# Optimization experiments

Hardware: AMD Instinct MI355X
Metric: run time of the kernel (lower is better)

The kernel has to match this reference:

```python
import jax, jax.numpy as jnp
import numpy as np

B, IN, H, NB = 8192, 1024, 2048, 8
BS = H // NB  # 256


def setup_inputs() -> dict:
    key = jax.random.key(0)
    ks = jax.random.split(key, 4)
    s = 0.02
    return {
        "x": jax.random.normal(ks[0], (B, IN), dtype=jnp.float32),
        "h": jax.random.normal(ks[1], (B, H), dtype=jnp.float32),
        "W_ir": jax.random.normal(ks[2], (3 * H, IN), dtype=jnp.float32) * s,
        "b_ir_lin": jnp.zeros((3 * H,), dtype=jnp.float32),
        "b_ir": jnp.zeros((3 * H,), dtype=jnp.float32),
        "W_h": jax.random.normal(ks[3], (NB, 3 * BS, BS), dtype=jnp.float32) * s,
        "b_hr": jnp.zeros((3 * H,), dtype=jnp.float32),
    }


def reference(x, h, W_ir, b_ir_lin, b_ir, W_h, b_hr):
    b = x.shape[0]
    nb, three_bs, bs = W_h.shape
    hdim = nb * bs
    # input projection: w_ir(x) + b_ir  -> [B, 3H], chunked globally into r,z,n
    wx = x @ W_ir.T + b_ir_lin + b_ir
    wxr, wxz, wxn = jnp.split(wx, 3, axis=1)
    wxr = wxr.reshape(b, nb, bs)
    wxz = wxz.reshape(b, nb, bs)
    wxn = wxn.reshape(b, nb, bs)
    # block-diagonal hidden projection: per-block Linear(bs -> 3*bs), no bias
    hb = h.reshape(b, nb, bs)
    # b_hr is sliced in contiguous chunks of 3*bs per block (local r,z,n layout)
    wh = jnp.einsum('bki,koi->bko', hb, W_h) + b_hr.reshape(nb, three_bs)
    whr, whz, whn = jnp.split(wh, 3, axis=2)
    r = jax.nn.sigmoid(wxr + whr)
    z = jax.nn.sigmoid(wxz + whz)
    n = jnp.tanh(wxn + r * whn)
    h_new = (1.0 - z) * hb + z * n
    return h_new.reshape(b, hdim)
```

## Files before the change

### kernel.cpp

```cpp
#include <hip/hip_runtime.h>
#include <cstdint>
#include <cstddef>


typedef __attribute__((ext_vector_type(8))) short bf16x8;
typedef __attribute__((ext_vector_type(4))) float f32x4;

__device__ __forceinline__ unsigned short f2bf(float f) {
    uint32_t u = __float_as_uint(f);
    u += 0x7FFFu + ((u >> 16) & 1u);
    return (unsigned short)(u >> 16);
}

__device__ __forceinline__ void gload16(const void* g, void* l) {
    __builtin_amdgcn_global_load_lds(
        (const __attribute__((address_space(1))) void*)g,
        (__attribute__((address_space(3))) void*)l,
        16, 0, 0);
}

__device__ __forceinline__ float sigmoidf_(float x) {
    return 1.0f / (1.0f + __expf(-x));
}
__device__ __forceinline__ float tanhf_(float x) {
    float e = __expf(-2.0f * fabsf(x));
    float t = (1.0f - e) / (1.0f + e);
    return copysignf(t, x);
}

__global__ __launch_bounds__(256)
void cast_f32_to_bf16(const float* __restrict__ s, unsigned short* __restrict__ d, int n4) {
    int i = blockIdx.x * 256 + threadIdx.x;
    if (i >= n4) return;
    const float4 v = *reinterpret_cast<const float4*>(s + (size_t)i * 4);
    ushort4 o;
    o.x = f2bf(v.x); o.y = f2bf(v.y); o.z = f2bf(v.z); o.w = f2bf(v.w);
    *reinterpret_cast<ushort4*>(d + (size_t)i * 4) = o;
}


#define MFMA12(mb, NT) do {                                                    \
    asm volatile("s_waitcnt lgkmcnt(0)" ::: "memory");                         \
    __builtin_amdgcn_sched_barrier(0);                                         \
    __builtin_amdgcn_s_setprio(1);                                             \
    _Pragma("unroll")                                                          \
    for (int m_ = 0; m_ < 4; ++m_) {                                           \
        acc[0][(mb) + m_] = __builtin_amdgcn_mfma_f32_16x16x32_bf16(           \
            av[m_], bv[0], acc[0][(mb) + m_], 0, 0, 0);                        \
        acc[1][(mb) + m_] = __builtin_amdgcn_mfma_f32_16x16x32_bf16(           \
            av[m_], bv[1], acc[1][(mb) + m_], 0, 0, 0);                        \
        acc[NT][(mb) + m_] = __builtin_amdgcn_mfma_f32_16x16x32_bf16(          \
            av[m_], bv[2], acc[NT][(mb) + m_], 0, 0, 0);                       \
    }                                                                          \
    __builtin_amdgcn_s_setprio(0);                                             \
} while (0)

#define LDA(m, kb_) (*(const bf16x8*)(aS + (wm * 128 + (m) * 16 + fr) * 64 + (kb_)))
#define LDB(s, kb_) (*(const bf16x8*)(bS + ((s) * 64 + wn * 16 + fr) * 64 + (kb_)))

#define IB1(kt, ds) do {                                                       \
    gload16(b1[0] + (size_t)(kt) * 64, Bs + (ds) * 12288 + doff);              \
    gload16(b1[1] + (size_t)(kt) * 64, Bs + (ds) * 12288 + 4096 + doff);       \
    gload16(b1[2] + (size_t)(kt) * 64, Bs + (ds) * 12288 + 8192 + doff); } while (0)
#define IA1a(kt, ds) do {                                                      \
    gload16(a1[0] + (size_t)(kt) * 64, As + (ds) * 16384 + doff);              \
    gload16(a1[2] + (size_t)(kt) * 64, As + (ds) * 16384 + 8192 + doff); } while (0)
#define IA1b(kt, ds) do {                                                      \
    gload16(a1[1] + (size_t)(kt) * 64, As + (ds) * 16384 + 4096 + doff);       \
    gload16(a1[3] + (size_t)(kt) * 64, As + (ds) * 16384 + 12288 + doff); } while (0)
#define IB2(k2, ds) do {                                                       \
    gload16(b2[0] + (size_t)(k2) * 64, Bs + (ds) * 12288 + doff);              \
    gload16(b2[1] + (size_t)(k2) * 64, Bs + (ds) * 12288 + 4096 + doff);       \
    gload16(b2[2] + (size_t)(k2) * 64, Bs + (ds) * 12288 + 8192 + doff); } while (0)
#define IA2a(k2, ds) do {                                                      \
    gload16(a2[0] + (size_t)(k2) * 64, As + (ds) * 16384 + doff);              \
    gload16(a2[2] + (size_t)(k2) * 64, As + (ds) * 16384 + 8192 + doff); } while (0)
#define IA2b(k2, ds) do {                                                      \
    gload16(a2[1] + (size_t)(k2) * 64, As + (ds) * 16384 + 4096 + doff);       \
    gload16(a2[3] + (size_t)(k2) * 64, As + (ds) * 16384 + 12288 + doff); } while (0)

#define KSTEP(slot_, I0, W0, I1, W1, I2, NT) do {                              \
    const unsigned short* aS = As + (slot_) * 16384;                           \
    const unsigned short* bS = Bs + (slot_) * 12288;                           \
    I0;                                                                        \
    asm volatile("s_waitcnt vmcnt(" W0 ")" ::: "memory");                      \
    __builtin_amdgcn_s_barrier();                                              \
    _Pragma("unroll") for (int m_ = 0; m_ < 4; ++m_) av[m_] = LDA(m_, kb0);    \
    _Pragma("unroll") for (int s_ = 0; s_ < 3; ++s_) bv[s_] = LDB(s_, kb0);    \
    MFMA12(0, NT);                                                             \
    I1;                                                                        \
    asm volatile("s_waitcnt vmcnt(" W1 ")" ::: "memory");                      \
    __builtin_amdgcn_s_barrier();                                              \
    _Pragma("unroll") for (int m_ = 0; m_ < 4; ++m_) av[m_] = LDA(4 + m_, kb0);\
    MFMA12(4, NT);                                                             \
    I2;                                                                        \
    _Pragma("unroll") for (int m_ = 0; m_ < 4; ++m_) av[m_] = LDA(m_, kb1);    \
    _Pragma("unroll") for (int s_ = 0; s_ < 3; ++s_) bv[s_] = LDB(s_, kb1);    \
    MFMA12(0, NT);                                                             \
    _Pragma("unroll") for (int m_ = 0; m_ < 4; ++m_) av[m_] = LDA(4 + m_, kb1);\
    MFMA12(4, NT);                                                             \
    __builtin_amdgcn_s_barrier();                                              \
} while (0)

__global__ __launch_bounds__(512, 2)
void gru_fused(const unsigned short* __restrict__ Xb,
               const unsigned short* __restrict__ Wirb,
               const unsigned short* __restrict__ Hbb,
               const unsigned short* __restrict__ Whb,
               const float* __restrict__ b_ir_lin,
               const float* __restrict__ b_ir,
               const float* __restrict__ b_hr,
               const float* __restrict__ Hf,
               float* __restrict__ out) {
    constexpr int K1 = 1024, H = 2048;
    __shared__ unsigned short lds[2 * 16384 + 2 * 12288];
    unsigned short* const As = lds;
    unsigned short* const Bs = lds + 2 * 16384;

    const int tid  = threadIdx.x;
    const int lane = tid & 63;
    const int w    = tid >> 6;
    const int wm   = w >> 2;
    const int wn   = w & 3;

    const int bid  = blockIdx.x;
    const int kb   = bid & 7;
    const int idx  = bid >> 3;
    const int bm   = (idx >> 2) * 256;
    const int hsub = idx & 3;
    const int hcb  = kb * 256 + hsub * 64;

    const int srow  = tid >> 3;
    const int chunk = (tid & 7) ^ (srow & 7);
    const int scol  = chunk * 8;
    const int doff  = tid * 8;
    const unsigned short* a1[4];
    const unsigned short* a2[4];
    #pragma unroll
    for (int s = 0; s < 4; ++s) {
        a1[s] = Xb  + (size_t)(bm + s * 64 + srow) * K1 + scol;
        a2[s] = Hbb + (size_t)(bm + s * 64 + srow) * H + kb * 256 + scol;
    }
    const unsigned short* b1[3];
    const unsigned short* b2[3];
    #pragma unroll
    for (int s = 0; s < 3; ++s) {
        b1[s] = Wirb + (size_t)(s * 2048 + hcb + srow) * K1 + scol;
        b2[s] = Whb + (size_t)kb * 196608 + (size_t)(s * 256 + hsub * 64 + srow) * 256 + scol;
    }

    const int fr  = lane & 15;
    const int k0e = (lane >> 4) * 8;
    const int mfr = (fr & 7) << 4;
    const int kb0 = ((k0e * 2) ^ mfr) >> 1;
    const int kb1 = (((k0e * 2) + 64) ^ mfr) >> 1;

    f32x4 acc[4][8] = {};
    bf16x8 av[4], bv[3];

    IB1(0, 0); IA1a(0, 0); IA1b(0, 0);

    #pragma unroll 1
    for (int t = 0; t < 15; ++t) {
        const int sl = t & 1, nx = sl ^ 1;
        KSTEP(sl, IB1(t + 1, nx), "5", IA1a(t + 1, nx), "5", IA1b(t + 1, nx), 2);
    }
    KSTEP(1, IB2(0, 0), "5", IA2a(0, 0), "5", IA2b(0, 0), 2);
    #pragma unroll 1
    for (int t = 16; t < 19; ++t) {
        const int sl = t & 1, nx = sl ^ 1;
        KSTEP(sl, IB2(t - 15, nx), "5", IA2a(t - 15, nx), "5", IA2b(t - 15, nx), 3);
    }
    KSTEP(1, ((void)0), "2", ((void)0), "0", ((void)0), 3);

    const int rq   = (lane >> 4) * 4;
    const int hcol = hcb + wn * 16 + fr;
    const int lcol = hcol & 255;
    const float bir0 = b_ir_lin[hcol]        + b_ir[hcol];
    const float bir1 = b_ir_lin[2048 + hcol] + b_ir[2048 + hcol];
    const float bir2 = b_ir_lin[4096 + hcol] + b_ir[4096 + hcol];
    const float bhr0 = b_hr[kb * 768 + lcol];
    const float bhr1 = b_hr[kb * 768 + 256 + lcol];
    const float bhr2 = b_hr[kb * 768 + 512 + lcol];
    #pragma unroll
    for (int mi = 0; mi < 8; ++mi) {
        #pragma unroll
        for (int r = 0; r < 4; ++r) {
            const int row = bm + wm * 128 + mi * 16 + rq + r;
            const float pr = acc[0][mi][r] + bir0 + bhr0;
            const float pz = acc[1][mi][r] + bir1 + bhr1;
            const float xn = acc[2][mi][r] + bir2;
            const float hn = acc[3][mi][r] + bhr2;
            const float rg = sigmoidf_(pr);
            const float zg = sigmoidf_(pz);
            const float ng = tanhf_(xn + rg * hn);
            const float hv = Hf[(size_t)row * H + hcol];
            out[(size_t)row * H + hcol] = (1.0f - zg) * hv + zg * ng;
        }
    }
}

extern "C" void kernel_launch(void* const* d_in, const int* in_sizes, int n_in,
                              void* d_out, int out_size, void* d_ws, size_t ws_size,
                              hipStream_t stream) {
    const float* x        = (const float*)d_in[0];
    const float* h        = (const float*)d_in[1];
    const float* W_ir     = (const float*)d_in[2];
    const float* b_ir_lin = (const float*)d_in[3];
    const float* b_ir     = (const float*)d_in[4];
    const float* W_h      = (const float*)d_in[5];
    const float* b_hr     = (const float*)d_in[6];
    float* out = (float*)d_out;

    char* ws = (char*)d_ws;
    unsigned short* xb   = (unsigned short*)(ws);
    unsigned short* wirb = (unsigned short*)(ws + 16777216);
    unsigned short* hb   = (unsigned short*)(ws + 29360128);
    unsigned short* whb  = (unsigned short*)(ws + 62914560);

    cast_f32_to_bf16<<<8192,  256, 0, stream>>>(x,    xb,   2097152);
    cast_f32_to_bf16<<<6144,  256, 0, stream>>>(W_ir, wirb, 1572864);
    cast_f32_to_bf16<<<16384, 256, 0, stream>>>(h,    hb,   4194304);
    cast_f32_to_bf16<<<1536,  256, 0, stream>>>(W_h,  whb,  393216);

    gru_fused<<<1024, 512, 0, stream>>>(xb, wirb, hb, whb,
                                        b_ir_lin, b_ir, b_hr, h, out);
}
```

Measured before the change: 182.1 us.

## Halve fused GRU block tile to 128 rows with 256-thread blocks

Changes the fused GEMM+GRU kernel from 512-thread blocks covering 256 batch rows to 256-thread blocks covering 128 rows, doubling the grid to 2048 blocks. Each wave now computes a 64x32 sub-tile (4 M fragments by 2 N fragments per gate) instead of 128x16, and the global-to-LDS load schedule is regrouped into three phases with a single wait and barrier per phase pair. The aim is smaller LDS use per block, more blocks in flight and better wave load balance. In exchange, each weight tile is reloaded by twice as many blocks, which raises weight traffic per output element.

Measured after the change: 177.6 us. -2.5%, faster.

```diff
diff --git a/kernel.cpp b/kernel.cpp
--- a/kernel.cpp
+++ b/kernel.cpp
@@ -39,70 +39,74 @@
 }
 
 
-#define MFMA12(mb, NT) do {                                                    \
+#define MFMA12(n_, NT) do {                                                    \
     asm volatile("s_waitcnt lgkmcnt(0)" ::: "memory");                         \
     __builtin_amdgcn_sched_barrier(0);                                         \
     __builtin_amdgcn_s_setprio(1);                                             \
     _Pragma("unroll")                                                          \
     for (int m_ = 0; m_ < 4; ++m_) {                                           \
-        acc[0][(mb) + m_] = __builtin_amdgcn_mfma_f32_16x16x32_bf16(           \
-            av[m_], bv[0], acc[0][(mb) + m_], 0, 0, 0);                        \
-        acc[1][(mb) + m_] = __builtin_amdgcn_mfma_f32_16x16x32_bf16(           \
-            av[m_], bv[1], acc[1][(mb) + m_], 0, 0, 0);                        \
-        acc[NT][(mb) + m_] = __builtin_amdgcn_mfma_f32_16x16x32_bf16(          \
-            av[m_], bv[2], acc[NT][(mb) + m_], 0, 0, 0);                       \
+        acc[0][m_][n_] = __builtin_amdgcn_mfma_f32_16x16x32_bf16(              \
+            av[m_], bv[0], acc[0][m_][n_], 0, 0, 0);                           \
+        acc[1][m_][n_] = __builtin_amdgcn_mfma_f32_16x16x32_bf16(              \
+            av[m_], bv[1], acc[1][m_][n_], 0, 0, 0);                           \
+        acc[NT][m_][n_] = __builtin_amdgcn_mfma_f32_16x16x32_bf16(             \
+            av[m_], bv[2], acc[NT][m_][n_], 0, 0, 0);                          \
     }                                                                          \
     __builtin_amdgcn_s_setprio(0);                                             \
 } while (0)
 
-#define LDA(m, kb_) (*(const bf16x8*)(aS + (wm * 128 + (m) * 16 + fr) * 64 + (kb_)))
-#define LDB(s, kb_) (*(const bf16x8*)(bS + ((s) * 64 + wn * 16 + fr) * 64 + (kb_)))
-
-#define IB1(kt, ds) do {                                                       \
-    gload16(b1[0] + (size_t)(kt) * 64, Bs + (ds) * 12288 + doff);              \
-    gload16(b1[1] + (size_t)(kt) * 64, Bs + (ds) * 12288 + 4096 + doff);       \
-    gload16(b1[2] + (size_t)(kt) * 64, Bs + (ds) * 12288 + 8192 + doff); } while (0)
-#define IA1a(kt, ds) do {                                                      \
-    gload16(a1[0] + (size_t)(kt) * 64, As + (ds) * 16384 + doff);              \
-    gload16(a1[2] + (size_t)(kt) * 64, As + (ds) * 16384 + 8192 + doff); } while (0)
-#define IA1b(kt, ds) do {                                                      \
-    gload16(a1[1] + (size_t)(kt) * 64, As + (ds) * 16384 + 4096 + doff);       \
-    gload16(a1[3] + (size_t)(kt) * 64, As + (ds) * 16384 + 12288 + doff); } while (0)
-#define IB2(k2, ds) do {                                                       \
-    gload16(b2[0] + (size_t)(k2) * 64, Bs + (ds) * 12288 + doff);              \
-    gload16(b2[1] + (size_t)(k2) * 64, Bs + (ds) * 12288 + 4096 + doff);       \
-    gload16(b2[2] + (size_t)(k2) * 64, Bs + (ds) * 12288 + 8192 + doff); } while (0)
-#define IA2a(k2, ds) do {                                                      \
-    gload16(a2[0] + (size_t)(k2) * 64, As + (ds) * 16384 + doff);              \
-    gload16(a2[2] + (size_t)(k2) * 64, As + (ds) * 16384 + 8192 + doff); } while (0)
-#define IA2b(k2, ds) do {                                                      \
-    gload16(a2[1] + (size_t)(k2) * 64, As + (ds) * 16384 + 4096 + doff);       \
-    gload16(a2[3] + (size_t)(k2) * 64, As + (ds) * 16384 + 12288 + doff); } while (0)
-
-#define KSTEP(slot_, I0, W0, I1, W1, I2, NT) do {                              \
-    const unsigned short* aS = As + (slot_) * 16384;                           \
+#define LDA(m, kb_) (*(const bf16x8*)(aS + (wm * 64 + (m) * 16 + fr) * 64 + (kb_)))
+#define LDB(s, n_, kb_) (*(const bf16x8*)(bS + ((s) * 64 + wn * 32 + (n_) * 16 + fr) * 64 + (kb_)))
+
+#define I0_1(kt, ds) do {                                                      \
+    gload16(b1[0] + (size_t)(kt) * 64, Bs + (ds) * 12288 + 0 * 2048 + doff);   \
+    gload16(b1[1] + (size_t)(kt) * 64, Bs + (ds) * 12288 + 1 * 2048 + doff);   \
+    gload16(b1[2] + (size_t)(kt) * 64, Bs + (ds) * 12288 + 2 * 2048 + doff);   \
+    gload16(b1[3] + (size_t)(kt) * 64, Bs + (ds) * 12288 + 3 * 2048 + doff); } while (0)
+#define I1_1(kt, ds) do {                                                      \
+    gload16(b1[4] + (size_t)(kt) * 64, Bs + (ds) * 12288 + 4 * 2048 + doff);   \
+    gload16(b1[5] + (size_t)(kt) * 64, Bs + (ds) * 12288 + 5 * 2048 + doff);   \
+    gload16(a1[0] + (size_t)(kt) * 64, As + (ds) * 8192 + 0 * 2048 + doff);    \
+    gload16(a1[1] + (size_t)(kt) * 64, As + (ds) * 8192 + 1 * 2048 + doff); } while (0)
+#define I2_1(kt, ds) do {                                                      \
+    gload16(a1[2] + (size_t)(kt) * 64, As + (ds) * 8192 + 2 * 2048 + doff);    \
+    gload16(a1[3] + (size_t)(kt) * 64, As + (ds) * 8192 + 3 * 2048 + doff); } while (0)
+#define I0_2(k2, ds) do {                                                      \
+    gload16(b2[0] + (size_t)(k2) * 64, Bs + (ds) * 12288 + 0 * 2048 + doff);   \
+    gload16(b2[1] + (size_t)(k2) * 64, Bs + (ds) * 12288 + 1 * 2048 + doff);   \
+    gload16(b2[2] + (size_t)(k2) * 64, Bs + (ds) * 12288 + 2 * 2048 + doff);   \
+    gload16(b2[3] + (size_t)(k2) * 64, Bs + (ds) * 12288 + 3 * 2048 + doff); } while (0)
+#define I1_2(k2, ds) do {                                                      \
+    gload16(b2[4] + (size_t)(k2) * 64, Bs + (ds) * 12288 + 4 * 2048 + doff);   \
+    gload16(b2[5] + (size_t)(k2) * 64, Bs + (ds) * 12288 + 5 * 2048 + doff);   \
+    gload16(a2[0] + (size_t)(k2) * 64, As + (ds) * 8192 + 0 * 2048 + doff);    \
+    gload16(a2[1] + (size_t)(k2) * 64, As + (ds) * 8192 + 1 * 2048 + doff); } while (0)
+#define I2_2(k2, ds) do {                                                      \
+    gload16(a2[2] + (size_t)(k2) * 64, As + (ds) * 8192 + 2 * 2048 + doff);    \
+    gload16(a2[3] + (size_t)(k2) * 64, As + (ds) * 8192 + 3 * 2048 + doff); } while (0)
+
+#define KSTEP(slot_, I0, W0, I1, I2, NT) do {                                  \
+    const unsigned short* aS = As + (slot_) * 8192;                            \
     const unsigned short* bS = Bs + (slot_) * 12288;                           \
     I0;                                                                        \
     asm volatile("s_waitcnt vmcnt(" W0 ")" ::: "memory");                      \
     __builtin_amdgcn_s_barrier();                                              \
     _Pragma("unroll") for (int m_ = 0; m_ < 4; ++m_) av[m_] = LDA(m_, kb0);    \
-    _Pragma("unroll") for (int s_ = 0; s_ < 3; ++s_) bv[s_] = LDB(s_, kb0);    \
+    _Pragma("unroll") for (int s_ = 0; s_ < 3; ++s_) bv[s_] = LDB(s_, 0, kb0); \
     MFMA12(0, NT);                                                             \
     I1;                                                                        \
-    asm volatile("s_waitcnt vmcnt(" W1 ")" ::: "memory");                      \
-    __builtin_amdgcn_s_barrier();                                              \
-    _Pragma("unroll") for (int m_ = 0; m_ < 4; ++m_) av[m_] = LDA(4 + m_, kb0);\
-    MFMA12(4, NT);                                                             \
+    _Pragma("unroll") for (int s_ = 0; s_ < 3; ++s_) bv[s_] = LDB(s_, 1, kb0); \
+    MFMA12(1, NT);                                                             \
     I2;                                                                        \
     _Pragma("unroll") for (int m_ = 0; m_ < 4; ++m_) av[m_] = LDA(m_, kb1);    \
-    _Pragma("unroll") for (int s_ = 0; s_ < 3; ++s_) bv[s_] = LDB(s_, kb1);    \
+    _Pragma("unroll") for (int s_ = 0; s_ < 3; ++s_) bv[s_] = LDB(s_, 0, kb1); \
     MFMA12(0, NT);                                                             \
-    _Pragma("unroll") for (int m_ = 0; m_ < 4; ++m_) av[m_] = LDA(4 + m_, kb1);\
-    MFMA12(4, NT);                                                             \
+    _Pragma("unroll") for (int s_ = 0; s_ < 3; ++s_) bv[s_] = LDB(s_, 1, kb1); \
+    MFMA12(1, NT);                                                             \
     __builtin_amdgcn_s_barrier();                                              \
 } while (0)
 
-__global__ __launch_bounds__(512, 2)
+__global__ __launch_bounds__(256, 2)
 void gru_fused(const unsigned short* __restrict__ Xb,
                const unsigned short* __restrict__ Wirb,
                const unsigned short* __restrict__ Hbb,
@@ -113,20 +117,20 @@
                const float* __restrict__ Hf,
                float* __restrict__ out) {
     constexpr int K1 = 1024, H = 2048;
-    __shared__ unsigned short lds[2 * 16384 + 2 * 12288];
+    __shared__ unsigned short lds[2 * 8192 + 2 * 12288];
     unsigned short* const As = lds;
-    unsigned short* const Bs = lds + 2 * 16384;
+    unsigned short* const Bs = lds + 2 * 8192;
 
     const int tid  = threadIdx.x;
     const int lane = tid & 63;
     const int w    = tid >> 6;
-    const int wm   = w >> 2;
-    const int wn   = w & 3;
+    const int wm   = w >> 1;
+    const int wn   = w & 1;
 
     const int bid  = blockIdx.x;
     const int kb   = bid & 7;
     const int idx  = bid >> 3;
-    const int bm   = (idx >> 2) * 256;
+    const int bm   = (idx >> 2) * 128;
     const int hsub = idx & 3;
     const int hcb  = kb * 256 + hsub * 64;
 
@@ -137,16 +141,18 @@
     const unsigned short* a1[4];
     const unsigned short* a2[4];
     #pragma unroll
-    for (int s = 0; s < 4; ++s) {
-        a1[s] = Xb  + (size_t)(bm + s * 64 + srow) * K1 + scol;
-        a2[s] = Hbb + (size_t)(bm + s * 64 + srow) * H + kb * 256 + scol;
-    }
-    const unsigned short* b1[3];
-    const unsigned short* b2[3];
+    for (int q = 0; q < 4; ++q) {
+        a1[q] = Xb  + (size_t)(bm + q * 32 + srow) * K1 + scol;
+        a2[q] = Hbb + (size_t)(bm + q * 32 + srow) * H + kb * 256 + scol;
+    }
+    const unsigned short* b1[6];
+    const unsigned short* b2[6];
     #pragma unroll
-    for (int s = 0; s < 3; ++s) {
-        b1[s] = Wirb + (size_t)(s * 2048 + hcb + srow) * K1 + scol;
-        b2[s] = Whb + (size_t)kb * 196608 + (size_t)(s * 256 + hsub * 64 + srow) * 256 + scol;
+    for (int q = 0; q < 6; ++q) {
+        const int s  = q >> 1;
+        const int rr = (q & 1) * 32 + srow;
+        b1[q] = Wirb + (size_t)(s * 2048 + hcb + rr) * K1 + scol;
+        b2[q] = Whb + (size_t)kb * 196608 + (size_t)(s * 256 + hsub * 64 + rr) * 256 + scol;
     }
 
     const int fr  = lane & 15;
@@ -155,47 +161,50 @@
     const int kb0 = ((k0e * 2) ^ mfr) >> 1;
     const int kb1 = (((k0e * 2) + 64) ^ mfr) >> 1;
 
-    f32x4 acc[4][8] = {};
+    f32x4 acc[4][4][2] = {};
     bf16x8 av[4], bv[3];
 
-    IB1(0, 0); IA1a(0, 0); IA1b(0, 0);
+    I0_1(0, 0); I1_1(0, 0); I2_1(0, 0);
 
     #pragma unroll 1
     for (int t = 0; t < 15; ++t) {
         const int sl = t & 1, nx = sl ^ 1;
-        KSTEP(sl, IB1(t + 1, nx), "5", IA1a(t + 1, nx), "5", IA1b(t + 1, nx), 2);
-    }
-    KSTEP(1, IB2(0, 0), "5", IA2a(0, 0), "5", IA2b(0, 0), 2);
+        KSTEP(sl, I0_1(t + 1, nx), "4", I1_1(t + 1, nx), I2_1(t + 1, nx), 2);
+    }
+    KSTEP(1, I0_2(0, 0), "4", I1_2(0, 0), I2_2(0, 0), 2);
     #pragma unroll 1
     for (int t = 16; t < 19; ++t) {
         const int sl = t & 1, nx = sl ^ 1;
-        KSTEP(sl, IB2(t - 15, nx), "5", IA2a(t - 15, nx), "5", IA2b(t - 15, nx), 3);
-    }
-    KSTEP(1, ((void)0), "2", ((void)0), "0", ((void)0), 3);
-
-    const int rq   = (lane >> 4) * 4;
-    const int hcol = hcb + wn * 16 + fr;
-    const int lcol = hcol & 255;
-    const float bir0 = b_ir_lin[hcol]        + b_ir[hcol];
-    const float bir1 = b_ir_lin[2048 + hcol] + b_ir[2048 + hcol];
-    const float bir2 = b_ir_lin[4096 + hcol] + b_ir[4096 + hcol];
-    const float bhr0 = b_hr[kb * 768 + lcol];
-    const float bhr1 = b_hr[kb * 768 + 256 + lcol];
-    const float bhr2 = b_hr[kb * 768 + 512 + lcol];
+        KSTEP(sl, I0_2(t - 15, nx), "4", I1_2(t - 15, nx), I2_2(t - 15, nx), 3);
+    }
+    KSTEP(1, ((void)0), "0", ((void)0), ((void)0), 3);
+
+    const int rq = (lane >> 4) * 4;
     #pragma unroll
-    for (int mi = 0; mi < 8; ++mi) {
+    for (int n = 0; n < 2; ++n) {
+        const int hcol = hcb + wn * 32 + n * 16 + fr;
+        const int lcol = hcol & 255;
+        const float bir0 = b_ir_lin[hcol]        + b_ir[hcol];
+        const float bir1 = b_ir_lin[2048 + hcol] + b_ir[2048 + hcol];
+        const float bir2 = b_ir_lin[4096 + hcol] + b_ir[4096 + hcol];
+        const float bhr0 = b_hr[kb * 768 + lcol];
+        const float bhr1 = b_hr[kb * 768 + 256 + lcol];
+        const float bhr2 = b_hr[kb * 768 + 512 + lcol];
         #pragma unroll
-        for (int r = 0; r < 4; ++r) {
-            const int row = bm + wm * 128 + mi * 16 + rq + r;
-            const float pr = acc[0][mi][r] + bir0 + bhr0;
-            const float pz = acc[1][mi][r] + bir1 + bhr1;
-            const float xn = acc[2][mi][r] + bir2;
-            const float hn = acc[3][mi][r] + bhr2;
-            const float rg = sigmoidf_(pr);
-            const float zg = sigmoidf_(pz);
-            const float ng = tanhf_(xn + rg * hn);
-            const float hv = Hf[(size_t)row * H + hcol];
-            out[(size_t)row * H + hcol] = (1.0f - zg) * hv + zg * ng;
+        for (int mi = 0; mi < 4; ++mi) {
+            #pragma unroll
+            for (int r = 0; r < 4; ++r) {
+                const int row = bm + wm * 64 + mi * 16 + rq + r;
+                const float pr = acc[0][mi][n][r] + bir0 + bhr0;
+                const float pz = acc[1][mi][n][r] + bir1 + bhr1;
+                const float xn = acc[2][mi][n][r] + bir2;
+                const float hn = acc[3][mi][n][r] + bhr2;
+                const float rg = sigmoidf_(pr);
+                const float zg = sigmoidf_(pz);
+                const float ng = tanhf_(xn + rg * hn);
+                const float hv = Hf[(size_t)row * H + hcol];
+                out[(size_t)row * H + hcol] = (1.0f - zg) * hv + zg * ng;
+            }
         }
     }
 }
@@ -223,6 +232,6 @@
     cast_f32_to_bf16<<<16384, 256, 0, stream>>>(h,    hb,   4194304);
     cast_f32_to_bf16<<<1536,  256, 0, stream>>>(W_h,  whb,  393216);
 
-    gru_fused<<<1024, 512, 0, stream>>>(xb, wirb, hb, whb,
+    gru_fused<<<2048, 256, 0, stream>>>(xb, wirb, hb, whb,
                                         b_ir_lin, b_ir, b_hr, h, out);
 }
```
